# Performance work log

Hardware: AMD Instinct MI355X
Metric: run time of the kernel (lower is better)

Reference implementation:

```python
import jax, jax.numpy as jnp
import numpy as np

BATCH, SEQ, DIM, HEADS, DSTATE, BLOCK = 2, 4096, 1024, 16, 64, 64
LN_EPS = 1e-6

def segsum(x):
    # x: (..., T) -> (..., T, T); segsum[i, j] = sum_{j < k <= i} x[k]; -inf above diagonal
    T = x.shape[-1]
    cs = jnp.cumsum(x, axis=-1)
    seg = cs[..., :, None] - cs[..., None, :]
    mask = jnp.tril(jnp.ones((T, T), dtype=bool))
    return jnp.where(mask, seg, -jnp.inf)

def ssd_minimal_discrete(X, A, C, B, block_len):
    # X: (b,s,h,p) already multiplied by dt; A: (b,s,h) = A*dt; C readout, B input: (b,s,h,n)
    b, s, h, p = X.shape
    n = B.shape[-1]
    c = s // block_len
    l = block_len
    Xc = X.reshape(b, c, l, h, p)
    Bc = B.reshape(b, c, l, h, n)
    Cc = C.reshape(b, c, l, h, n)
    Ac = A.reshape(b, c, l, h).transpose(0, 3, 1, 2)  # (b,h,c,l)
    A_cumsum = jnp.cumsum(Ac, axis=-1)
    # 1. intra-chunk (diagonal block) outputs
    L = jnp.exp(segsum(Ac))  # (b,h,c,l,l)
    Y_diag = jnp.einsum('bclhn,bcshn,bhcls,bcshp->bclhp', Cc, Bc, L, Xc)
    # 2. states at end of each chunk
    decay_states = jnp.exp(A_cumsum[..., -1:] - A_cumsum)
    states = jnp.einsum('bclhn,bhcl,bclhp->bchpn', Bc, decay_states, Xc)
    # 3. inter-chunk recurrence on chunk states
    init = jnp.zeros_like(states[:, :1])
    states = jnp.concatenate([init, states], axis=1)  # (b,c+1,h,p,n)
    decay_chunk = jnp.exp(segsum(jnp.pad(A_cumsum[..., -1], ((0, 0), (0, 0), (1, 0)))))
    new_states = jnp.einsum('bhzc,bchpn->bzhpn', decay_chunk, states)
    states, final_state = new_states[:, :-1], new_states[:, -1]
    # 4. state -> output contribution (off-diagonal blocks)
    state_decay_out = jnp.exp(A_cumsum)
    Y_off = jnp.einsum('bclhn,bchpn,bhcl->bclhp', Cc, states, state_decay_out)
    return (Y_diag + Y_off).reshape(b, s, h, p), final_state

def setup_inputs():
    key = jax.random.key(0)
    ks = jax.random.split(key, 8)
    X = jax.random.normal(ks[0], (BATCH, SEQ, DIM), jnp.float32)
    B = jax.random.normal(ks[1], (BATCH, SEQ, HEADS * DSTATE), jnp.float32)
    C = jax.random.normal(ks[2], (BATCH, SEQ, HEADS * DSTATE), jnp.float32)
    W_dt = jax.random.normal(ks[3], (DIM, HEADS), jnp.float32) * 0.02
    # dt_bias initializer: inverse-softplus of dt ~ LogUniform(1e-3, 1e-1)
    dt = jnp.exp(jax.random.uniform(ks[4], (1, SEQ, HEADS)) * (jnp.log(0.1) - jnp.log(0.001)) + jnp.log(0.001))
    dt = jnp.clip(dt, 1e-4)
    dt_bias = dt + jnp.log(-jnp.expm1(-dt))
    # a_log initializer: log of Uniform(1, 16)
    a_log = jnp.log(jax.random.uniform(ks[5], (HEADS,), minval=1.0, maxval=16.0))
    W_out = jax.random.normal(ks[6], (DIM, DIM), jnp.float32) * 0.02
    ln_scale = jnp.ones((DIM,), jnp.float32)
    ln_bias = jnp.zeros((DIM,), jnp.float32)
    return {"X": X, "B": B, "C": C, "W_dt": W_dt, "dt_bias": dt_bias, "a_log": a_log,
            "W_out": W_out, "ln_scale": ln_scale, "ln_bias": ln_bias, "block_len": BLOCK}

def reference(X, B, C, W_dt, dt_bias, a_log, W_out, ln_scale, ln_bias, block_len):
    b, s, dim = X.shape
    h = a_log.shape[0]
    Xh = X.reshape(b, s, h, -1)
    Bh = B.reshape(b, s, h, -1)
    Ch = C.reshape(b, s, h, -1)
    dt = jax.nn.softplus(jnp.einsum('bsd,dh->bsh', X, W_dt) + dt_bias)  # (b,s,h)
    A = -jnp.exp(a_log)  # (h,)
    y, final_state = ssd_minimal_discrete(Xh * dt[..., None], A * dt, Ch, Bh, block_len)
    y = y.reshape(b, s, dim)
    mu = jnp.mean(y, axis=-1, keepdims=True)
    var = jnp.mean(jnp.square(y - mu), axis=-1, keepdims=True)
    yn = (y - mu) / jnp.sqrt(var + LN_EPS) * ln_scale + ln_bias
    out = jnp.einsum('bsd,de->bse', yn, W_out)
    return out, final_state
```

## Files before the change

kernel.cpp:

```cpp
#include <hip/hip_runtime.h>
#include <hip/hip_bf16.h>
#include <hip/hip_fp16.h>
#include <math.h>

#define BATCH   2
#define SEQ     4096
#define DIM     1024
#define HEADS   16
#define DSTATE  64
#define HEADDIM 64
#define BLOCKL  64
#define NCHUNK  64
#define ROWS    (BATCH*SEQ)

typedef __attribute__((ext_vector_type(4))) float f32x4;
typedef __attribute__((ext_vector_type(8))) short bf16x8;
typedef __attribute__((ext_vector_type(8))) _Float16 f16x8;

static __device__ __forceinline__ float softplus_f(float x){
    return (x > 20.f) ? x : log1pf(__expf(x));
}
static __device__ __forceinline__ ushort f2b(float f){
    __hip_bfloat16 h = __float2bfloat16(f);
    return *reinterpret_cast<ushort*>(&h);
}
static __device__ __forceinline__ void gload16(const void* g, void* l){
    __builtin_amdgcn_global_load_lds((const __attribute__((address_space(1))) unsigned int*)g,
                                     (__attribute__((address_space(3))) unsigned int*)l, 16, 0, 0);
}

__global__ __launch_bounds__(256) void k_dt(const float* __restrict__ X,
        const float* __restrict__ Wdt, const float* __restrict__ dtb,
        const float* __restrict__ alog,
        float* __restrict__ dt_g, float* __restrict__ dtA_g){
    int r = blockIdx.x;
    int s = r & (SEQ-1);
    int tid = threadIdx.x;
    __shared__ float xrow[DIM];
    __shared__ float red[16][17];
    *(f32x4*)(xrow + tid*4) = *(const f32x4*)(X + (size_t)r*DIM + tid*4);
    __syncthreads();
    int part = tid >> 4, h = tid & 15;
    int d0 = part * 64;
    float acc = 0.f;
    #pragma unroll 8
    for (int i = 0; i < 64; ++i)
        acc += xrow[d0 + i] * Wdt[(size_t)(d0 + i)*HEADS + h];
    red[part][h] = acc;
    __syncthreads();
    if (tid < 16){
        float sum = 0.f;
        #pragma unroll
        for (int p = 0; p < 16; ++p) sum += red[p][tid];
        sum += dtb[(size_t)s*HEADS + tid];
        float dtv = softplus_f(sum);
        dt_g[(size_t)r*HEADS + tid]  = dtv;
        dtA_g[(size_t)r*HEADS + tid] = -__expf(alog[tid]) * dtv;
    }
}

__global__ __launch_bounds__(256) void k_chunk(const float* __restrict__ X,
        const float* __restrict__ Bin, const float* __restrict__ Cin,
        const float* __restrict__ dt_g, const float* __restrict__ dtA_g,
        float* __restrict__ y_g, ushort* __restrict__ cstate, float* __restrict__ css_g){
    int bid = blockIdx.x;
    int h = bid & 15, c = (bid >> 4) & 63, b = bid >> 10;
    int tid = threadIdx.x;
    int lane = tid & 63, wave = tid >> 6;
    int r0 = b*SEQ + c*BLOCKL;

    __shared__ __align__(16) char region0[18432];
    __shared__ __align__(16) ushort XdT [64*72];
    __shared__ __align__(16) ushort WXdT[64*72];
    __shared__ __align__(16) ushort BT  [64*72];
    __shared__ float csh[64], dtsh[64], wsh[64];
    ushort* Cs = (ushort*)region0;
    ushort* Bs = (ushort*)(region0 + 9216);
    float*  Mf = (float*)region0;

    int l  = tid >> 2;
    int c0 = (tid & 3) * 16;

    f32x4 xr[4], br[4], cr[4];
    {
        const float* xp = X   + (size_t)(r0 + l)*DIM + h*HEADDIM + c0;
        const float* bp = Bin + (size_t)(r0 + l)*DIM + h*DSTATE  + c0;
        const float* cp = Cin + (size_t)(r0 + l)*DIM + h*DSTATE  + c0;
        #pragma unroll
        for (int q = 0; q < 4; ++q){
            xr[q] = *(const f32x4*)(xp + q*4);
            br[q] = *(const f32x4*)(bp + q*4);
            cr[q] = *(const f32x4*)(cp + q*4);
        }
    }
    if (tid < 64){
        dtsh[tid] = dt_g[(size_t)(r0 + tid)*HEADS + h];
        float a = dtA_g[(size_t)(r0 + tid)*HEADS + h];
        #pragma unroll
        for (int off = 1; off < 64; off <<= 1){
            float v = __shfl_up(a, off, 64);
            if (tid >= off) a += v;
        }
        csh[tid] = a;
        css_g[(size_t)bid*64 + tid] = a;
        float cs63 = __shfl(a, 63, 64);
        wsh[tid] = __expf(cs63 - a);
    }
    ushort tc[16], tb[16];
    #pragma unroll
    for (int q = 0; q < 4; ++q)
        #pragma unroll
        for (int j = 0; j < 4; ++j){
            tc[q*4+j] = f2b(cr[q][j]);
            tb[q*4+j] = f2b(br[q][j]);
        }
    *(uint4*)&Cs[l*72 + c0]     = *(uint4*)&tc[0];
    *(uint4*)&Cs[l*72 + c0 + 8] = *(uint4*)&tc[8];
    *(uint4*)&Bs[l*72 + c0]     = *(uint4*)&tb[0];
    *(uint4*)&Bs[l*72 + c0 + 8] = *(uint4*)&tb[8];
    __syncthreads();

    {
        float dl = dtsh[l], wl = wsh[l];
        #pragma unroll
        for (int q = 0; q < 4; ++q)
            #pragma unroll
            for (int j = 0; j < 4; ++j){
                int p = c0 + q*4 + j;
                float xv = xr[q][j] * dl;
                XdT [p*72 + l] = f2b(xv);
                WXdT[p*72 + l] = f2b(xv * wl);
                BT  [p*72 + l] = tb[q*4+j];
            }
    }
    __syncthreads();

    int cl15  = lane & 15;
    int g     = lane >> 4;
    int arow  = wave*16 + cl15;
    int kof   = g * 8;
    int rbase = wave*16 + g*4;

    f32x4 gacc[4];
    #pragma unroll
    for (int j = 0; j < 4; ++j) gacc[j] = (f32x4){0.f,0.f,0.f,0.f};
    #pragma unroll
    for (int k = 0; k < 2; ++k){
        bf16x8 a = *(const bf16x8*)&Cs[arow*72 + k*32 + kof];
        #pragma unroll
        for (int j = 0; j < 4; ++j){
            bf16x8 bb = *(const bf16x8*)&Bs[(16*j + cl15)*72 + k*32 + kof];
            gacc[j] = __builtin_amdgcn_mfma_f32_16x16x32_bf16(a, bb, gacc[j], 0, 0, 0);
        }
    }
    __syncthreads();

    #pragma unroll
    for (int j = 0; j < 4; ++j){
        #pragma unroll
        for (int r = 0; r < 4; ++r){
            int row = rbase + r, col = 16*j + cl15;
            float m = 0.f;
            if (col <= row) m = gacc[j][r] * __expf(csh[row] - csh[col]);
            Mf[row*65 + col] = m;
        }
    }
    __syncthreads();

    f32x4 y[4];
    #pragma unroll
    for (int j = 0; j < 4; ++j) y[j] = (f32x4){0.f,0.f,0.f,0.f};
    #pragma unroll
    for (int k = 0; k < 2; ++k){
        bf16x8 am;
        #pragma unroll
        for (int i = 0; i < 8; ++i)
            am[i] = (short)f2b(Mf[arow*65 + k*32 + kof + i]);
        #pragma unroll
        for (int j = 0; j < 4; ++j){
            bf16x8 bx = *(const bf16x8*)&XdT[(16*j + cl15)*72 + k*32 + kof];
            y[j] = __builtin_amdgcn_mfma_f32_16x16x32_bf16(am, bx, y[j], 0, 0, 0);
        }
    }
    #pragma unroll
    for (int j = 0; j < 4; ++j)
        #pragma unroll
        for (int r = 0; r < 4; ++r)
            y_g[(size_t)(r0 + rbase + r)*DIM + h*HEADDIM + 16*j + cl15] = y[j][r];

    f32x4 st[4];
    #pragma unroll
    for (int j = 0; j < 4; ++j) st[j] = (f32x4){0.f,0.f,0.f,0.f};
    #pragma unroll
    for (int k = 0; k < 2; ++k){
        bf16x8 aw = *(const bf16x8*)&WXdT[arow*72 + k*32 + kof];
        #pragma unroll
        for (int j = 0; j < 4; ++j){
            bf16x8 bb = *(const bf16x8*)&BT[(16*j + cl15)*72 + k*32 + kof];
            st[j] = __builtin_amdgcn_mfma_f32_16x16x32_bf16(aw, bb, st[j], 0, 0, 0);
        }
    }
    #pragma unroll
    for (int j = 0; j < 4; ++j)
        #pragma unroll
        for (int r = 0; r < 4; ++r){
            __half hv = __float2half(st[j][r]);
            cstate[(size_t)bid*4096 + (size_t)(rbase + r)*64 + 16*j + cl15] = *(ushort*)&hv;
        }
}

__global__ __launch_bounds__(256) void k_scan(ushort* __restrict__ cstate,
        const float* __restrict__ css_g, float* __restrict__ fs_out){
    int bid = blockIdx.x;
    int tile = bid & 7, hh = (bid >> 3) & 15, b = bid >> 7;
    int pn = tile*512 + threadIdx.x*2;
    float P0 = 0.f, P1 = 0.f;
    for (int c = 0; c < NCHUNK; ++c){
        size_t base = (size_t)((b*NCHUNK + c)*HEADS + hh);
        float e = __expf(css_g[base*64 + 63]);
        __half2 cur = *(const __half2*)&cstate[base*4096 + pn];
        *( __half2*)&cstate[base*4096 + pn] = __floats2half2_rn(P0, P1);
        float2 cf = __half22float2(cur);
        P0 = e*P0 + cf.x;
        P1 = e*P1 + cf.y;
    }
    *(float2*)&fs_out[(size_t)(b*HEADS + hh)*4096 + pn] = make_float2(P0, P1);
}

__global__ __launch_bounds__(256) void k_yoff(const float* __restrict__ Cin,
        const ushort* __restrict__ cstate, const float* __restrict__ css_g,
        float* __restrict__ y_g){
    int bid = blockIdx.x;
    int h = bid & 15, c = (bid >> 4) & 63, b = bid >> 10;
    int tid = threadIdx.x;
    int lane = tid & 63, wave = tid >> 6;
    int r0 = b*SEQ + c*BLOCKL;
    __shared__ __align__(16) ushort Cs[64*72];
    __shared__ __align__(16) ushort Ss[64*72];
    __shared__ float cse[64];
    {
        int l  = tid >> 2;
        int c0 = (tid & 3) * 16;
        const float* cp = Cin + (size_t)(r0 + l)*DIM + h*DSTATE + c0;
        ushort tc[16];
        #pragma unroll
        for (int q = 0; q < 4; ++q){
            f32x4 vc = *(const f32x4*)(cp + q*4);
            #pragma unroll
            for (int j = 0; j < 4; ++j){
                __half hv = __float2half(vc[j]);
                tc[q*4+j] = *(ushort*)&hv;
            }
        }
        *(uint4*)&Cs[l*72 + c0]     = *(uint4*)&tc[0];
        *(uint4*)&Cs[l*72 + c0 + 8] = *(uint4*)&tc[8];
        const ushort* sp = cstate + (size_t)bid*4096 + (size_t)l*64 + c0;
        *(uint4*)&Ss[l*72 + c0]     = *(const uint4*)sp;
        *(uint4*)&Ss[l*72 + c0 + 8] = *(const uint4*)(sp + 8);
    }
    if (tid < 64) cse[tid] = __expf(css_g[(size_t)bid*64 + tid]);
    __syncthreads();

    int cl15 = lane & 15;
    int g    = lane >> 4;
    int arow = wave*16 + cl15;
    int kof  = g * 8;
    f32x4 acc[4];
    #pragma unroll
    for (int j = 0; j < 4; ++j) acc[j] = (f32x4){0.f,0.f,0.f,0.f};
    #pragma unroll
    for (int k = 0; k < 2; ++k){
        f16x8 a = *(const f16x8*)&Cs[arow*72 + k*32 + kof];
        #pragma unroll
        for (int j = 0; j < 4; ++j){
            f16x8 bb = *(const f16x8*)&Ss[(16*j + cl15)*72 + k*32 + kof];
            acc[j] = __builtin_amdgcn_mfma_f32_16x16x32_f16(a, bb, acc[j], 0, 0, 0);
        }
    }
    int rbase = wave*16 + g*4;
    #pragma unroll
    for (int j = 0; j < 4; ++j)
        #pragma unroll
        for (int r = 0; r < 4; ++r){
            float e = cse[rbase + r];
            float* yp = y_g + (size_t)(r0 + rbase + r)*DIM + h*HEADDIM + 16*j + cl15;
            *yp += e * acc[j][r];
        }
}

__global__ __launch_bounds__(256) void k_ln(const float* __restrict__ y_g,
        const float* __restrict__ scale, const float* __restrict__ bias,
        __hip_bfloat16* __restrict__ yn){
    int r = blockIdx.x, tid = threadIdx.x;
    const float* yp = y_g + (size_t)r*DIM;
    f32x4 v = *(const f32x4*)(yp + tid*4);
    float s1 = v.x + v.y + v.z + v.w;
    float s2 = v.x*v.x + v.y*v.y + v.z*v.z + v.w*v.w;
    #pragma unroll
    for (int m = 32; m > 0; m >>= 1){
        s1 += __shfl_xor(s1, m, 64);
        s2 += __shfl_xor(s2, m, 64);
    }
    __shared__ float w1[4], w2[4];
    int wv = tid >> 6;
    if ((tid & 63) == 0){ w1[wv] = s1; w2[wv] = s2; }
    __syncthreads();
    float S1 = w1[0]+w1[1]+w1[2]+w1[3];
    float S2 = w2[0]+w2[1]+w2[2]+w2[3];
    float mu  = S1 * (1.f/DIM);
    float var = S2 * (1.f/DIM) - mu*mu;
    float rstd = rsqrtf(var + 1e-6f);
    int d = tid*4;
    f32x4 sc = *(const f32x4*)(scale + d);
    f32x4 bi = *(const f32x4*)(bias + d);
    union { __hip_bfloat16 h[4]; short4 s4; } u;
    u.h[0] = __float2bfloat16((v.x - mu)*rstd*sc.x + bi.x);
    u.h[1] = __float2bfloat16((v.y - mu)*rstd*sc.y + bi.y);
    u.h[2] = __float2bfloat16((v.z - mu)*rstd*sc.z + bi.z);
    u.h[3] = __float2bfloat16((v.w - mu)*rstd*sc.w + bi.w);
    *(short4*)((short*)yn + (size_t)r*DIM + d) = u.s4;
}

__global__ __launch_bounds__(256) void k_wt(const float* __restrict__ W,
        __hip_bfloat16* __restrict__ Wt){
    __shared__ float t[64][65];
    int kt = blockIdx.x >> 4, nt = blockIdx.x & 15;
    int tid = threadIdx.x;
    int lr = tid >> 4, lc4 = (tid & 15) * 4;
    #pragma unroll
    for (int q = 0; q < 4; ++q){
        int k = lr + q*16;
        *(f32x4*)&t[k][lc4] = *(const f32x4*)(W + (size_t)(kt*64 + k)*DIM + nt*64 + lc4);
    }
    __syncthreads();
    #pragma unroll
    for (int q = 0; q < 4; ++q){
        int n = lr + q*16;
        union { __hip_bfloat16 h[4]; short4 s4; } u;
        #pragma unroll
        for (int j = 0; j < 4; ++j) u.h[j] = __float2bfloat16(t[lc4+j][n]);
        *(short4*)((short*)Wt + (size_t)(nt*64 + n)*DIM + kt*64 + lc4) = u.s4;
    }
}

__global__ __launch_bounds__(256) void k_gemm(const __hip_bfloat16* __restrict__ A,
        const __hip_bfloat16* __restrict__ Bt, float* __restrict__ Out){
    __shared__ __align__(16) ushort As[128*32];
    __shared__ __align__(16) ushort Bsh[128*32];
    int bid = blockIdx.x;
    int bn = bid & 7, bm = bid >> 3;
    int tid = threadIdx.x;
    int lane = tid & 63, wave = tid >> 6;
    int wr = wave >> 1, wc = wave & 1;
    f32x4 acc[4][4];
    #pragma unroll
    for (int i = 0; i < 4; ++i)
        #pragma unroll
        for (int j = 0; j < 4; ++j)
            acc[i][j] = (f32x4){0.f, 0.f, 0.f, 0.f};
    const ushort* Ag = (const ushort*)A  + (size_t)bm*128*1024;
    const ushort* Bg = (const ushort*)Bt + (size_t)bn*128*1024;
    int row0 = tid >> 2;
    int col0 = (tid & 3) * 8;
    for (int k0 = 0; k0 < 1024; k0 += 32){
        const ushort* sA = Ag + (size_t)row0*1024 + k0 + col0;
        const ushort* sB = Bg + (size_t)row0*1024 + k0 + col0;
        gload16(sA,           &As[row0*32 + col0]);
        gload16(sA + 64*1024, &As[(row0+64)*32 + col0]);
        gload16(sB,           &Bsh[row0*32 + col0]);
        gload16(sB + 64*1024, &Bsh[(row0+64)*32 + col0]);
        __syncthreads();
        bf16x8 af[4], bfr[4];
        #pragma unroll
        for (int i = 0; i < 4; ++i){
            int arow = wr*64 + i*16 + (lane & 15);
            af[i] = *(const bf16x8*)&As[arow*32 + ((lane >> 4) << 3)];
        }
        #pragma unroll
        for (int j = 0; j < 4; ++j){
            int brow = wc*64 + j*16 + (lane & 15);
            bfr[j] = *(const bf16x8*)&Bsh[brow*32 + ((lane >> 4) << 3)];
        }
        #pragma unroll
        for (int i = 0; i < 4; ++i)
            #pragma unroll
            for (int j = 0; j < 4; ++j)
                acc[i][j] = __builtin_amdgcn_mfma_f32_16x16x32_bf16(af[i], bfr[j], acc[i][j], 0, 0, 0);
        __syncthreads();
    }
    #pragma unroll
    for (int i = 0; i < 4; ++i){
        int m0 = bm*128 + wr*64 + i*16 + ((lane >> 4) << 2);
        #pragma unroll
        for (int j = 0; j < 4; ++j){
            int n = bn*128 + wc*64 + j*16 + (lane & 15);
            #pragma unroll
            for (int reg = 0; reg < 4; ++reg)
                Out[(size_t)(m0 + reg)*1024 + n] = acc[i][j][reg];
        }
    }
}

extern "C" void kernel_launch(void* const* d_in, const int* in_sizes, int n_in,
                              void* d_out, int out_size, void* d_ws, size_t ws_size,
                              hipStream_t stream){
    const float* X    = (const float*)d_in[0];
    const float* Bin  = (const float*)d_in[1];
    const float* Cin  = (const float*)d_in[2];
    const float* Wdt  = (const float*)d_in[3];
    const float* dtb  = (const float*)d_in[4];
    const float* alog = (const float*)d_in[5];
    const float* Wout = (const float*)d_in[6];
    const float* lns  = (const float*)d_in[7];
    const float* lnb  = (const float*)d_in[8];

    float* out = (float*)d_out;
    float* y_g = out;
    float* fs_out = out + (size_t)ROWS*DIM;

    float* dt_g   = (float*)d_ws;
    float* dtA_g  = dt_g  + 131072;
    float* css_g  = dtA_g + 131072;
    ushort* cstate = (ushort*)(css_g + 131072);
    __hip_bfloat16* yn = (__hip_bfloat16*)(cstate + 8388608);
    __hip_bfloat16* Wt = yn + (size_t)ROWS*DIM;

    k_dt   <<<ROWS,               256, 0, stream>>>(X, Wdt, dtb, alog, dt_g, dtA_g);
    k_chunk<<<BATCH*NCHUNK*HEADS, 256, 0, stream>>>(X, Bin, Cin, dt_g, dtA_g, y_g, cstate, css_g);
    k_scan <<<BATCH*HEADS*8,      256, 0, stream>>>(cstate, css_g, fs_out);
    k_yoff <<<BATCH*NCHUNK*HEADS, 256, 0, stream>>>(Cin, cstate, css_g, y_g);
    k_ln   <<<ROWS,               256, 0, stream>>>(y_g, lns, lnb, yn);
    k_wt   <<<256,                256, 0, stream>>>(Wout, Wt);
    k_gemm <<<512,                256, 0, stream>>>(yn, Wt, out);
}
```

Measured before the change: 131.8 us.

## Store intermediate y in bf16 and fold decay weights into B for chunk state

The intermediate SSM output y is now kept in a bf16 workspace buffer rather than fp32 in the output buffer. k_chunk writes it, k_yoff read-modify-writes it, and k_ln normalises it in place for the GEMM. This halves the traffic of those passes and drops the separate yn buffer. The chunk-state MFMA now reuses XdT and applies the decay weight to B instead of X, which removes one shared-memory transposed array and its stores. The cost is that y is rounded to bf16 before the off-diagonal contribution is added and before the layernorm statistics are taken, which adds extra rounding error.

```diff
diff --git a/kernel.cpp b/kernel.cpp
--- a/kernel.cpp
+++ b/kernel.cpp
@@ -23,6 +23,10 @@
 static __device__ __forceinline__ ushort f2b(float f){
     __hip_bfloat16 h = __float2bfloat16(f);
     return *reinterpret_cast<ushort*>(&h);
+}
+static __device__ __forceinline__ float b2f(ushort u){
+    uint x = ((uint)u) << 16;
+    return *reinterpret_cast<float*>(&x);
 }
 static __device__ __forceinline__ void gload16(const void* g, void* l){
     __builtin_amdgcn_global_load_lds((const __attribute__((address_space(1))) unsigned int*)g,
@@ -62,7 +66,7 @@
 __global__ __launch_bounds__(256) void k_chunk(const float* __restrict__ X,
         const float* __restrict__ Bin, const float* __restrict__ Cin,
         const float* __restrict__ dt_g, const float* __restrict__ dtA_g,
-        float* __restrict__ y_g, ushort* __restrict__ cstate, float* __restrict__ css_g){
+        ushort* __restrict__ ybf, ushort* __restrict__ cstate, float* __restrict__ css_g){
     int bid = blockIdx.x;
     int h = bid & 15, c = (bid >> 4) & 63, b = bid >> 10;
     int tid = threadIdx.x;
@@ -70,9 +74,8 @@
     int r0 = b*SEQ + c*BLOCKL;
 
     __shared__ __align__(16) char region0[18432];
-    __shared__ __align__(16) ushort XdT [64*72];
-    __shared__ __align__(16) ushort WXdT[64*72];
-    __shared__ __align__(16) ushort BT  [64*72];
+    __shared__ __align__(16) ushort XdT[64*72];
+    __shared__ __align__(16) ushort WBT[64*72];
     __shared__ float csh[64], dtsh[64], wsh[64];
     ushort* Cs = (ushort*)region0;
     ushort* Bs = (ushort*)(region0 + 9216);
@@ -127,10 +130,8 @@
             #pragma unroll
             for (int j = 0; j < 4; ++j){
                 int p = c0 + q*4 + j;
-                float xv = xr[q][j] * dl;
-                XdT [p*72 + l] = f2b(xv);
-                WXdT[p*72 + l] = f2b(xv * wl);
-                BT  [p*72 + l] = tb[q*4+j];
+                XdT[p*72 + l] = f2b(xr[q][j] * dl);
+                WBT[p*72 + l] = f2b(br[q][j] * wl);
             }
     }
     __syncthreads();
@@ -186,17 +187,17 @@
     for (int j = 0; j < 4; ++j)
         #pragma unroll
         for (int r = 0; r < 4; ++r)
-            y_g[(size_t)(r0 + rbase + r)*DIM + h*HEADDIM + 16*j + cl15] = y[j][r];
+            ybf[(size_t)(r0 + rbase + r)*DIM + h*HEADDIM + 16*j + cl15] = f2b(y[j][r]);
 
     f32x4 st[4];
     #pragma unroll
     for (int j = 0; j < 4; ++j) st[j] = (f32x4){0.f,0.f,0.f,0.f};
     #pragma unroll
     for (int k = 0; k < 2; ++k){
-        bf16x8 aw = *(const bf16x8*)&WXdT[arow*72 + k*32 + kof];
-        #pragma unroll
-        for (int j = 0; j < 4; ++j){
-            bf16x8 bb = *(const bf16x8*)&BT[(16*j + cl15)*72 + k*32 + kof];
+        bf16x8 aw = *(const bf16x8*)&XdT[arow*72 + k*32 + kof];
+        #pragma unroll
+        for (int j = 0; j < 4; ++j){
+            bf16x8 bb = *(const bf16x8*)&WBT[(16*j + cl15)*72 + k*32 + kof];
             st[j] = __builtin_amdgcn_mfma_f32_16x16x32_bf16(aw, bb, st[j], 0, 0, 0);
         }
     }
@@ -229,7 +230,7 @@
 
 __global__ __launch_bounds__(256) void k_yoff(const float* __restrict__ Cin,
         const ushort* __restrict__ cstate, const float* __restrict__ css_g,
-        float* __restrict__ y_g){
+        ushort* __restrict__ ybf){
     int bid = blockIdx.x;
     int h = bid & 15, c = (bid >> 4) & 63, b = bid >> 10;
     int tid = threadIdx.x;
@@ -283,19 +284,21 @@
         #pragma unroll
         for (int r = 0; r < 4; ++r){
             float e = cse[rbase + r];
-            float* yp = y_g + (size_t)(r0 + rbase + r)*DIM + h*HEADDIM + 16*j + cl15;
-            *yp += e * acc[j][r];
-        }
-}
-
-__global__ __launch_bounds__(256) void k_ln(const float* __restrict__ y_g,
-        const float* __restrict__ scale, const float* __restrict__ bias,
-        __hip_bfloat16* __restrict__ yn){
+            size_t idx = (size_t)(r0 + rbase + r)*DIM + h*HEADDIM + 16*j + cl15;
+            ybf[idx] = f2b(b2f(ybf[idx]) + e * acc[j][r]);
+        }
+}
+
+__global__ __launch_bounds__(256) void k_ln(ushort* __restrict__ ybf,
+        const float* __restrict__ scale, const float* __restrict__ bias){
     int r = blockIdx.x, tid = threadIdx.x;
-    const float* yp = y_g + (size_t)r*DIM;
-    f32x4 v = *(const f32x4*)(yp + tid*4);
-    float s1 = v.x + v.y + v.z + v.w;
-    float s2 = v.x*v.x + v.y*v.y + v.z*v.z + v.w*v.w;
+    ushort* yp = ybf + (size_t)r*DIM + tid*4;
+    short4 raw = *(const short4*)yp;
+    float v[4];
+    v[0] = b2f((ushort)raw.x); v[1] = b2f((ushort)raw.y);
+    v[2] = b2f((ushort)raw.z); v[3] = b2f((ushort)raw.w);
+    float s1 = v[0]+v[1]+v[2]+v[3];
+    float s2 = v[0]*v[0]+v[1]*v[1]+v[2]*v[2]+v[3]*v[3];
     #pragma unroll
     for (int m = 32; m > 0; m >>= 1){
         s1 += __shfl_xor(s1, m, 64);
@@ -313,12 +316,11 @@
     int d = tid*4;
     f32x4 sc = *(const f32x4*)(scale + d);
     f32x4 bi = *(const f32x4*)(bias + d);
-    union { __hip_bfloat16 h[4]; short4 s4; } u;
-    u.h[0] = __float2bfloat16((v.x - mu)*rstd*sc.x + bi.x);
-    u.h[1] = __float2bfloat16((v.y - mu)*rstd*sc.y + bi.y);
-    u.h[2] = __float2bfloat16((v.z - mu)*rstd*sc.z + bi.z);
-    u.h[3] = __float2bfloat16((v.w - mu)*rstd*sc.w + bi.w);
-    *(short4*)((short*)yn + (size_t)r*DIM + d) = u.s4;
+    ushort o[4];
+    #pragma unroll
+    for (int j = 0; j < 4; ++j)
+        o[j] = f2b((v[j] - mu)*rstd*sc[j] + bi[j]);
+    *(short4*)yp = *(short4*)&o[0];
 }
 
 __global__ __launch_bounds__(256) void k_wt(const float* __restrict__ W,
@@ -415,21 +417,20 @@
     const float* lnb  = (const float*)d_in[8];
 
     float* out = (float*)d_out;
-    float* y_g = out;
     float* fs_out = out + (size_t)ROWS*DIM;
 
     float* dt_g   = (float*)d_ws;
     float* dtA_g  = dt_g  + 131072;
     float* css_g  = dtA_g + 131072;
     ushort* cstate = (ushort*)(css_g + 131072);
-    __hip_bfloat16* yn = (__hip_bfloat16*)(cstate + 8388608);
-    __hip_bfloat16* Wt = yn + (size_t)ROWS*DIM;
+    ushort* ybf    = cstate + 8388608;
+    __hip_bfloat16* Wt = (__hip_bfloat16*)(ybf + 8388608);
 
     k_dt   <<<ROWS,               256, 0, stream>>>(X, Wdt, dtb, alog, dt_g, dtA_g);
-    k_chunk<<<BATCH*NCHUNK*HEADS, 256, 0, stream>>>(X, Bin, Cin, dt_g, dtA_g, y_g, cstate, css_g);
+    k_chunk<<<BATCH*NCHUNK*HEADS, 256, 0, stream>>>(X, Bin, Cin, dt_g, dtA_g, ybf, cstate, css_g);
     k_scan <<<BATCH*HEADS*8,      256, 0, stream>>>(cstate, css_g, fs_out);
-    k_yoff <<<BATCH*NCHUNK*HEADS, 256, 0, stream>>>(Cin, cstate, css_g, y_g);
-    k_ln   <<<ROWS,               256, 0, stream>>>(y_g, lns, lnb, yn);
+    k_yoff <<<BATCH*NCHUNK*HEADS, 256, 0, stream>>>(Cin, cstate, css_g, ybf);
+    k_ln   <<<ROWS,               256, 0, stream>>>(ybf, lns, lnb);
     k_wt   <<<256,                256, 0, stream>>>(Wout, Wt);
-    k_gemm <<<512,                256, 0, stream>>>(yn, Wt, out);
-}
+    k_gemm <<<512,                256, 0, stream>>>((const __hip_bfloat16*)ybf, Wt, out);
+}
```

New measurement: 127.0 us. 3.6% less time.
